# Performance work log

Hardware: AMD Instinct MI355X
Metric: run time of the kernel (lower is better)

Reference implementation:

```python
import jax, jax.numpy as jnp
import numpy as np

N_STEPS = 20
ALPHA, BETA = 0.9, 0.8  # synaptic / membrane decay (unused given zero carried state, kept for clarity)


def _lcn_spiking_layer(h, knn, w, b):
    """h: [N, d_in]; knn: [d_out, K] indices into d_in; w: [d_out, K]; b: [1, d_out].
    Gather K neighbors per output node, weight, reduce, then snntorch Synaptic
    update with zero carried state (the source never stores returned syn/mem):
      syn = ALPHA*0 + I = I ; reset = (prev_mem > thr) = 0 ; mem = BETA*0 + syn - 0 = I
    and the layer output is mem (the source keeps the 3rd return value)."""
    g = h[:, knn]                                  # [N, d_out, K] irregular gather
    cur = jnp.sum(g * w[None, :, :], axis=2) + b   # [N, d_out]
    syn = ALPHA * jnp.zeros_like(cur) + cur
    mem = BETA * jnp.zeros_like(cur) + syn         # reset term is zero
    return mem


def setup_inputs() -> dict:
    key = jax.random.key(0)
    B, T, IN_DIM, K, OUT = 32, N_STEPS, 14400, 25, 2
    dims = [7200, 3600, 1800, 900, 450]
    ks = jax.random.split(key, 13)
    inp = {"x": jax.random.normal(ks[0], (B, T, IN_DIM), dtype=jnp.float32)}
    prev = IN_DIM
    for i, d in enumerate(dims):
        inp[f"w{i}"] = jax.random.normal(ks[1 + i], (d, K), dtype=jnp.float32) * (2.0 / K) ** 0.5
        inp[f"b{i}"] = jnp.zeros((1, d), dtype=jnp.float32)
        inp[f"knn{i}"] = jax.random.randint(ks[6 + i], (d, K), 0, prev)
        prev = d
    inp["Wfc"] = jax.random.normal(ks[11], (dims[-1], OUT), dtype=jnp.float32) * (1.0 / dims[-1]) ** 0.5
    inp["bfc"] = jnp.zeros((OUT,), dtype=jnp.float32)
    return inp


def reference(x, w0, w1, w2, w3, w4, b0, b1, b2, b3, b4, Wfc, bfc,
              knn0, knn1, knn2, knn3, knn4):
    # Source loops over 20 timesteps with independent (state never carried) work;
    # fold time into batch to vectorize, then keep the last step's angle only,
    # exactly matching the returned value of the torch forward.
    B, T, D = x.shape
    h = x.reshape(B * T, D)
    layers = ((w0, b0, knn0), (w1, b1, knn1), (w2, b2, knn2), (w3, b3, knn3), (w4, b4, knn4))
    for w, b, knn in layers:
        h = _lcn_spiking_layer(h, knn, w, b)
    angle = h @ Wfc + bfc                     # [B*T, out_dim]
    angle = angle.reshape(B, T, -1)[:, -1]    # last timestep, as in the source
    return angle
```

## Files before the change

### kernel.cpp

```cpp
#include <hip/hip_runtime.h>


#define ROWS 32
#define TSTEPS 20
#define D0 14400
#define D1 7200
#define D2 3600
#define D3 1800
#define D4 900
#define D5 450
#define KNB 25

__global__ __launch_bounds__(256)
void l0_stage(const float* __restrict__ x, float* __restrict__ h1,
              const float* __restrict__ w, const float* __restrict__ bvec,
              const int* __restrict__ knn)
{
    __shared__ float s[D0];
    const int r = blockIdx.y;
    const float* xrow = x + ((size_t)r * TSTEPS + (TSTEPS - 1)) * (size_t)D0;

    const float4* src = reinterpret_cast<const float4*>(xrow);
    float4* dst = reinterpret_cast<float4*>(s);
#pragma unroll 1
    for (int i = threadIdx.x; i < D0 / 4; i += 256)
        dst[i] = src[i];
    __syncthreads();

    const int j0 = blockIdx.x * 900;
#pragma unroll 1
    for (int j = j0 + threadIdx.x; j < j0 + 900; j += 256) {
        const int*   kn = knn + j * KNB;
        const float* ww = w   + j * KNB;
        float acc = bvec[j];
#pragma unroll
        for (int k = 0; k < KNB; ++k)
            acc += s[kn[k]] * ww[k];
        h1[(size_t)r * D1 + j] = acc;
    }
}

__global__ __launch_bounds__(1024)
void tail_fused(const float* __restrict__ h1,
                const float* __restrict__ w1, const float* __restrict__ b1, const int* __restrict__ n1,
                const float* __restrict__ w2, const float* __restrict__ b2, const int* __restrict__ n2,
                const float* __restrict__ w3, const float* __restrict__ b3, const int* __restrict__ n3,
                const float* __restrict__ w4, const float* __restrict__ b4, const int* __restrict__ n4,
                const float* __restrict__ Wfc, const float* __restrict__ bfc,
                float* __restrict__ out)
{
    __shared__ float sa[D1];
    __shared__ float sb[D2];
    __shared__ float sc[D3];
    __shared__ float sd[D4];
    __shared__ float se[D5];
    __shared__ float red[2];

    const int r   = blockIdx.x;
    const int tid = threadIdx.x;

    {
        const float4* src = reinterpret_cast<const float4*>(h1 + (size_t)r * D1);
        float4* dst = reinterpret_cast<float4*>(sa);
#pragma unroll 1
        for (int i = tid; i < D1 / 4; i += 1024)
            dst[i] = src[i];
    }
    __syncthreads();

#pragma unroll 1
    for (int j = tid; j < D2; j += 1024) {
        const int*   kn = n1 + j * KNB;
        const float* ww = w1 + j * KNB;
        float acc = b1[j];
#pragma unroll
        for (int k = 0; k < KNB; ++k)
            acc += sa[kn[k]] * ww[k];
        sb[j] = acc;
    }
    __syncthreads();

#pragma unroll 1
    for (int j = tid; j < D3; j += 1024) {
        const int*   kn = n2 + j * KNB;
        const float* ww = w2 + j * KNB;
        float acc = b2[j];
#pragma unroll
        for (int k = 0; k < KNB; ++k)
            acc += sb[kn[k]] * ww[k];
        sc[j] = acc;
    }
    __syncthreads();

#pragma unroll 1
    for (int j = tid; j < D4; j += 1024) {
        const int*   kn = n3 + j * KNB;
        const float* ww = w3 + j * KNB;
        float acc = b3[j];
#pragma unroll
        for (int k = 0; k < KNB; ++k)
            acc += sc[kn[k]] * ww[k];
        sd[j] = acc;
    }
    __syncthreads();

#pragma unroll 1
    for (int j = tid; j < D5; j += 1024) {
        const int*   kn = n4 + j * KNB;
        const float* ww = w4 + j * KNB;
        float acc = b4[j];
#pragma unroll
        for (int k = 0; k < KNB; ++k)
            acc += sd[kn[k]] * ww[k];
        se[j] = acc;
    }
    __syncthreads();

    if (tid == 0) { red[0] = bfc[0]; red[1] = bfc[1]; }

    float c0 = 0.0f, c1 = 0.0f;
#pragma unroll 1
    for (int j = tid; j < D5; j += 1024) {
        const float v = se[j];
        c0 += v * Wfc[2 * j + 0];
        c1 += v * Wfc[2 * j + 1];
    }
#pragma unroll
    for (int off = 32; off > 0; off >>= 1) {
        c0 += __shfl_down(c0, off);
        c1 += __shfl_down(c1, off);
    }
    __syncthreads();
    if ((tid & 63) == 0) {
        atomicAdd(&red[0], c0);
        atomicAdd(&red[1], c1);
    }
    __syncthreads();
    if (tid < 2)
        out[2 * r + tid] = red[tid];
}

extern "C" void kernel_launch(void* const* d_in, const int* in_sizes, int n_in,
                              void* d_out, int out_size, void* d_ws, size_t ws_size,
                              hipStream_t stream)
{
    const float* x    = (const float*)d_in[0];
    const float* w0   = (const float*)d_in[1];
    const float* b0   = (const float*)d_in[2];
    const int*   knn0 = (const int*)  d_in[3];
    const float* w1   = (const float*)d_in[4];
    const float* b1   = (const float*)d_in[5];
    const int*   knn1 = (const int*)  d_in[6];
    const float* w2   = (const float*)d_in[7];
    const float* b2   = (const float*)d_in[8];
    const int*   knn2 = (const int*)  d_in[9];
    const float* w3   = (const float*)d_in[10];
    const float* b3   = (const float*)d_in[11];
    const int*   knn3 = (const int*)  d_in[12];
    const float* w4   = (const float*)d_in[13];
    const float* b4   = (const float*)d_in[14];
    const int*   knn4 = (const int*)  d_in[15];
    const float* Wfc  = (const float*)d_in[16];
    const float* bfc  = (const float*)d_in[17];
    float* out = (float*)d_out;

    float* h1 = (float*)d_ws;

    l0_stage<<<dim3(D1 / 900, ROWS), dim3(256), 0, stream>>>(x, h1, w0, b0, knn0);

    tail_fused<<<dim3(ROWS), dim3(1024), 0, stream>>>(
        h1,
        w1, b1, knn1,
        w2, b2, knn2,
        w3, b3, knn3,
        w4, b4, knn4,
        Wfc, bfc, out);
}
```

Measured before the change: 138.7 us.

## Split layer 1 into wide transposed-layout kernel, shrink tail fused block

Layer 0 now writes its output transposed (node-major, 32 rows per node) so a new standalone layer-1 kernel can spread its work over 450 blocks. In that kernel each half-wavefront handles one output node across all 32 rows, which makes the gathered reads coalesced. Before this, layer 1 ran inside a 32-block tail kernel that used little of the GPU. The remaining tail kernel handles layers 2-4 plus the FC with 512 threads, and it loads its input from the transposed buffer with strided reads. The cost is one extra kernel launch and a global round trip for h2.

```diff
diff --git a/kernel.cpp b/kernel.cpp
--- a/kernel.cpp
+++ b/kernel.cpp
@@ -12,7 +12,7 @@
 #define KNB 25
 
 __global__ __launch_bounds__(256)
-void l0_stage(const float* __restrict__ x, float* __restrict__ h1,
+void l0_stage(const float* __restrict__ x, float* __restrict__ h1t,
               const float* __restrict__ w, const float* __restrict__ bvec,
               const int* __restrict__ knn)
 {
@@ -36,101 +36,103 @@
 #pragma unroll
         for (int k = 0; k < KNB; ++k)
             acc += s[kn[k]] * ww[k];
-        h1[(size_t)r * D1 + j] = acc;
+        h1t[(j << 5) + r] = acc;
     }
 }
 
-__global__ __launch_bounds__(1024)
-void tail_fused(const float* __restrict__ h1,
-                const float* __restrict__ w1, const float* __restrict__ b1, const int* __restrict__ n1,
+__global__ __launch_bounds__(256)
+void layer_t_k(const float* __restrict__ pin, float* __restrict__ pout,
+               const float* __restrict__ w, const float* __restrict__ bvec,
+               const int* __restrict__ knn, int npairs)
+{
+    const int lane = threadIdx.x & 63;
+    const int r  = lane & 31;
+    const int jj = lane >> 5;
+    const int nw = gridDim.x << 2;
+#pragma unroll 1
+    for (int jp = (blockIdx.x << 2) + (threadIdx.x >> 6); jp < npairs; jp += nw) {
+        const int j = (jp << 1) + jj;
+        const int*   kn = knn + j * KNB;
+        const float* ww = w   + j * KNB;
+        float acc = bvec[j];
+#pragma unroll
+        for (int k = 0; k < KNB; ++k)
+            acc += pin[(kn[k] << 5) + r] * ww[k];
+        pout[(j << 5) + r] = acc;
+    }
+}
+
+__global__ __launch_bounds__(512)
+void tail_fused(const float* __restrict__ h2t,
                 const float* __restrict__ w2, const float* __restrict__ b2, const int* __restrict__ n2,
                 const float* __restrict__ w3, const float* __restrict__ b3, const int* __restrict__ n3,
                 const float* __restrict__ w4, const float* __restrict__ b4, const int* __restrict__ n4,
                 const float* __restrict__ Wfc, const float* __restrict__ bfc,
                 float* __restrict__ out)
 {
-    __shared__ float sa[D1];
-    __shared__ float sb[D2];
-    __shared__ float sc[D3];
-    __shared__ float sd[D4];
-    __shared__ float se[D5];
+    __shared__ float s2[D2];
+    __shared__ float s3[D3];
+    __shared__ float s4[D4];
+    __shared__ float s5[D5];
     __shared__ float red[2];
 
     const int r   = blockIdx.x;
     const int tid = threadIdx.x;
 
-    {
-        const float4* src = reinterpret_cast<const float4*>(h1 + (size_t)r * D1);
-        float4* dst = reinterpret_cast<float4*>(sa);
 #pragma unroll 1
-        for (int i = tid; i < D1 / 4; i += 1024)
-            dst[i] = src[i];
-    }
+    for (int j = tid; j < D2; j += 512)
+        s2[j] = h2t[(j << 5) + r];
     __syncthreads();
 
 #pragma unroll 1
-    for (int j = tid; j < D2; j += 1024) {
-        const int*   kn = n1 + j * KNB;
-        const float* ww = w1 + j * KNB;
-        float acc = b1[j];
-#pragma unroll
-        for (int k = 0; k < KNB; ++k)
-            acc += sa[kn[k]] * ww[k];
-        sb[j] = acc;
-    }
-    __syncthreads();
-
-#pragma unroll 1
-    for (int j = tid; j < D3; j += 1024) {
+    for (int j = tid; j < D3; j += 512) {
         const int*   kn = n2 + j * KNB;
         const float* ww = w2 + j * KNB;
         float acc = b2[j];
 #pragma unroll
         for (int k = 0; k < KNB; ++k)
-            acc += sb[kn[k]] * ww[k];
-        sc[j] = acc;
+            acc += s2[kn[k]] * ww[k];
+        s3[j] = acc;
     }
     __syncthreads();
 
 #pragma unroll 1
-    for (int j = tid; j < D4; j += 1024) {
+    for (int j = tid; j < D4; j += 512) {
         const int*   kn = n3 + j * KNB;
         const float* ww = w3 + j * KNB;
         float acc = b3[j];
 #pragma unroll
         for (int k = 0; k < KNB; ++k)
-            acc += sc[kn[k]] * ww[k];
-        sd[j] = acc;
+            acc += s3[kn[k]] * ww[k];
+        s4[j] = acc;
     }
     __syncthreads();
 
 #pragma unroll 1
-    for (int j = tid; j < D5; j += 1024) {
+    for (int j = tid; j < D5; j += 512) {
         const int*   kn = n4 + j * KNB;
         const float* ww = w4 + j * KNB;
         float acc = b4[j];
 #pragma unroll
         for (int k = 0; k < KNB; ++k)
-            acc += sd[kn[k]] * ww[k];
-        se[j] = acc;
+            acc += s4[kn[k]] * ww[k];
+        s5[j] = acc;
     }
+
+    if (tid == 0) { red[0] = bfc[0]; red[1] = bfc[1]; }
     __syncthreads();
 
-    if (tid == 0) { red[0] = bfc[0]; red[1] = bfc[1]; }
-
     float c0 = 0.0f, c1 = 0.0f;
-#pragma unroll 1
-    for (int j = tid; j < D5; j += 1024) {
-        const float v = se[j];
-        c0 += v * Wfc[2 * j + 0];
-        c1 += v * Wfc[2 * j + 1];
+    if (tid < D5) {
+        const float v = s5[tid];
+        c0 = v * Wfc[2 * tid + 0];
+        c1 = v * Wfc[2 * tid + 1];
     }
 #pragma unroll
     for (int off = 32; off > 0; off >>= 1) {
         c0 += __shfl_down(c0, off);
         c1 += __shfl_down(c1, off);
     }
-    __syncthreads();
     if ((tid & 63) == 0) {
         atomicAdd(&red[0], c0);
         atomicAdd(&red[1], c1);
@@ -164,13 +166,15 @@
     const float* bfc  = (const float*)d_in[17];
     float* out = (float*)d_out;
 
-    float* h1 = (float*)d_ws;
+    float* h1t = (float*)d_ws;
+    float* h2t = h1t + (size_t)D1 * ROWS;
 
-    l0_stage<<<dim3(D1 / 900, ROWS), dim3(256), 0, stream>>>(x, h1, w0, b0, knn0);
+    l0_stage<<<dim3(D1 / 900, ROWS), dim3(256), 0, stream>>>(x, h1t, w0, b0, knn0);
 
-    tail_fused<<<dim3(ROWS), dim3(1024), 0, stream>>>(
-        h1,
-        w1, b1, knn1,
+    layer_t_k<<<dim3(450), dim3(256), 0, stream>>>(h1t, h2t, w1, b1, knn1, D2 / 2);
+
+    tail_fused<<<dim3(ROWS), dim3(512), 0, stream>>>(
+        h2t,
         w2, b2, knn2,
         w3, b3, knn3,
         w4, b4, knn4,
```

Measured after the change: 134.0 us. 1.03x faster.
